# Optimization experiments

Hardware: AMD Instinct MI355X
Metric: run time of the kernel (lower is better)

Reference implementation:

```python
import jax, jax.numpy as jnp
import numpy as np

N_TOKENS = 16384  # b * seq_len
D_MODEL = 4096
NUM_EXPERTS = 64
TOP_K = 2
EPS = 1e-8


def setup_inputs() -> dict:
    key = jax.random.key(0)
    kx, kw = jax.random.split(key)
    x = jax.random.normal(kx, (N_TOKENS, D_MODEL), dtype=jnp.float32)
    # nn.Linear weight: [num_experts, d_model], scaled like torch default init
    W = jax.random.normal(kw, (NUM_EXPERTS, D_MODEL), dtype=jnp.float32) / jnp.sqrt(D_MODEL)
    return {"x": x, "W": W}


def reference(x, W):
    # logits: [n_tokens, num_experts]
    logits = jnp.einsum('nd,ed->ne', x, W)
    scores = jax.nn.softmax(logits, axis=-1)
    topk_scores, topk_indices = jax.lax.top_k(scores, TOP_K)
    topk_scores = topk_scores / jnp.sum(topk_scores, axis=-1, keepdims=True)
    expert_prob = jnp.mean(scores, axis=0)  # [num_experts]
    load_balancing_loss = jnp.sum(expert_prob * jnp.log(expert_prob + EPS))
    return topk_scores, topk_indices, load_balancing_loss
```

## Files before the change

kernel.cpp:

```cpp
#include <hip/hip_runtime.h>
#include <hip/hip_bf16.h>

#define NT 16384
#define DM 4096
#define NE 64
#define MB 64
#define BK 128
#define NST (DM / BK)
#define LROW 132

typedef __attribute__((ext_vector_type(8))) short bf16x8;
typedef __attribute__((ext_vector_type(4))) float f32x4;

__device__ __forceinline__ unsigned short bf16_rne(float f) {
  const unsigned u = __float_as_uint(f);
  return (unsigned short)((u + 0x7FFFu + ((u >> 16) & 1u)) >> 16);
}

__device__ __forceinline__ void split2(float fa, float fb, unsigned& hp, unsigned& lp) {
  union { __hip_bfloat162 h; unsigned u; } cv;
  cv.h = __float22bfloat162_rn(make_float2(fa, fb));
  hp = cv.u;
  const float ha = __uint_as_float(hp << 16);
  const float hb = __uint_as_float(hp & 0xFFFF0000u);
  cv.h = __float22bfloat162_rn(make_float2(fa - ha, fb - hb));
  lp = cv.u;
}

__device__ __forceinline__ void splitA(const float4& c0, const float4& c1,
                                       bf16x8& hi, bf16x8& lo) {
  union { unsigned u[4]; bf16x8 v; } H, L;
  split2(c0.x, c0.y, H.u[0], L.u[0]);
  split2(c0.z, c0.w, H.u[1], L.u[1]);
  split2(c1.x, c1.y, H.u[2], L.u[2]);
  split2(c1.z, c1.w, H.u[3], L.u[3]);
  hi = H.v; lo = L.v;
}

__global__ void w_convert(const float* __restrict__ W,
                          unsigned short* __restrict__ Whi,
                          unsigned short* __restrict__ Wlo) {
  const int id   = blockIdx.x * 256 + threadIdx.x;
  const int lane = id & 63;
  const int nt   = (id >> 6) & 3;
  const int ks   = id >> 8;
  const float* src = W + (size_t)(nt * 16 + (lane & 15)) * DM + ks * 32 + (lane >> 4) * 8;
  unsigned short h[8], l[8];
#pragma unroll
  for (int j = 0; j < 8; ++j) {
    const float f = src[j];
    h[j] = bf16_rne(f);
    l[j] = bf16_rne(f - __uint_as_float((unsigned)h[j] << 16));
  }
  uint4 ph, pl;
  ph.x = h[0] | ((unsigned)h[1] << 16); ph.y = h[2] | ((unsigned)h[3] << 16);
  ph.z = h[4] | ((unsigned)h[5] << 16); ph.w = h[6] | ((unsigned)h[7] << 16);
  pl.x = l[0] | ((unsigned)l[1] << 16); pl.y = l[2] | ((unsigned)l[3] << 16);
  pl.z = l[4] | ((unsigned)l[5] << 16); pl.w = l[6] | ((unsigned)l[7] << 16);
  *(uint4*)(Whi + (size_t)id * 8) = ph;
  *(uint4*)(Wlo + (size_t)id * 8) = pl;
}

__launch_bounds__(512, 2)
__global__ void moe_mfma(const float* __restrict__ x,
                         const unsigned short* __restrict__ Whi,
                         const unsigned short* __restrict__ Wlo,
                         float* __restrict__ out,
                         float* __restrict__ bsum) {
  __shared__ float xs[2][MB][LROW];
  __shared__ float esums[8][NE];
  float* lg = &xs[0][0][0];

  const int tid  = threadIdx.x;
  const int lane = tid & 63;
  const int wv   = tid >> 6;
  const int wvu  = __builtin_amdgcn_readfirstlane(wv);
  const int tg   = wvu >> 1;
  const int eg   = wvu & 1;
  const int blk  = blockIdx.x;
  const int tok0 = blk * MB;

  const int srow = tid >> 3;
  const int scol = (tid & 7) * 4;
  const float* xrow = x + (size_t)(tok0 + srow) * DM + scol;

  float4 g0, g1, g2, g3;
#define LOADSTAGE(s) {                                        \
    const float* p = xrow + (size_t)(s) * BK;                 \
    g0 = *(const float4*)(p);                                 \
    g1 = *(const float4*)(p + 32);                            \
    g2 = *(const float4*)(p + 64);                            \
    g3 = *(const float4*)(p + 96); }
#define WRITESTAGE(b) {                                       \
    float* q = &xs[b][srow][scol];                            \
    *(float4*)(q)      = g0;                                  \
    *(float4*)(q + 32) = g1;                                  \
    *(float4*)(q + 64) = g2;                                  \
    *(float4*)(q + 96) = g3; }

  const unsigned short* bhp = Whi + (size_t)(eg * 2) * 512 + lane * 8;
  const unsigned short* blp = Wlo + (size_t)(eg * 2) * 512 + lane * 8;
  bf16x8 Bh0[2], Bl0[2], Bh1[2], Bl1[2];
#define LOADB(BH, BL, gk) {                                   \
    const size_t o = (size_t)(gk) * 2048;                     \
    BH[0] = *(const bf16x8*)(bhp + o);                        \
    BH[1] = *(const bf16x8*)(bhp + o + 512);                  \
    BL[0] = *(const bf16x8*)(blp + o);                        \
    BL[1] = *(const bf16x8*)(blp + o + 512); }

  const int arow = tg * 16 + (lane & 15);
  const int acol = (lane >> 4) * 8;

  f32x4 acc0 = (f32x4){0.f, 0.f, 0.f, 0.f};
  f32x4 acc1 = (f32x4){0.f, 0.f, 0.f, 0.f};

#define STEP(b, kk, BH, BL) {                                                          \
    const float* ap = &xs[b][arow][acol + (kk) * 32];                                  \
    const float4 f0 = *(const float4*)(ap);                                            \
    const float4 f1 = *(const float4*)(ap + 4);                                        \
    bf16x8 ah, al;                                                                     \
    splitA(f0, f1, ah, al);                                                            \
    acc0 = __builtin_amdgcn_mfma_f32_16x16x32_bf16(al, BL[0], acc0, 0, 0, 0);          \
    acc0 = __builtin_amdgcn_mfma_f32_16x16x32_bf16(al, BH[0], acc0, 0, 0, 0);          \
    acc0 = __builtin_amdgcn_mfma_f32_16x16x32_bf16(ah, BL[0], acc0, 0, 0, 0);          \
    acc0 = __builtin_amdgcn_mfma_f32_16x16x32_bf16(ah, BH[0], acc0, 0, 0, 0);          \
    acc1 = __builtin_amdgcn_mfma_f32_16x16x32_bf16(al, BL[1], acc1, 0, 0, 0);          \
    acc1 = __builtin_amdgcn_mfma_f32_16x16x32_bf16(al, BH[1], acc1, 0, 0, 0);          \
    acc1 = __builtin_amdgcn_mfma_f32_16x16x32_bf16(ah, BL[1], acc1, 0, 0, 0);          \
    acc1 = __builtin_amdgcn_mfma_f32_16x16x32_bf16(ah, BH[1], acc1, 0, 0, 0); }

  LOADSTAGE(0);
  LOADB(Bh0, Bl0, 0);
  WRITESTAGE(0);
  __syncthreads();

  for (int s = 0; s < NST; ++s) {
    const int b = s & 1;
    if (s + 1 < NST) LOADSTAGE(s + 1);
    const int g4 = s * 4;
    const int n1 = g4 + 1, n2 = g4 + 2, n3 = g4 + 3;
    const int n4 = (g4 + 4 < 128) ? g4 + 4 : 127;
    LOADB(Bh1, Bl1, n1); STEP(b, 0, Bh0, Bl0);
    LOADB(Bh0, Bl0, n2); STEP(b, 1, Bh1, Bl1);
    LOADB(Bh1, Bl1, n3); STEP(b, 2, Bh0, Bl0);
    LOADB(Bh0, Bl0, n4); STEP(b, 3, Bh1, Bl1);
    if (s + 1 < NST) WRITESTAGE((s + 1) & 1);
    __syncthreads();
  }

#pragma unroll
  for (int r = 0; r < 4; ++r) {
    const int t = tg * 16 + (lane >> 4) * 4 + r;
    lg[t * 65 + eg * 32 + (lane & 15)]      = acc0[r];
    lg[t * 65 + eg * 32 + 16 + (lane & 15)] = acc1[r];
  }
  __syncthreads();

  float esum = 0.f;
#pragma unroll
  for (int ti = 0; ti < 8; ++ti) {
    const int t = wvu * 8 + ti;
    const float lgv = lg[t * 65 + lane];

    float m = lgv;
#pragma unroll
    for (int off = 32; off; off >>= 1) m = fmaxf(m, __shfl_xor(m, off, 64));
    const float p = __expf(lgv - m);
    float Z = p;
#pragma unroll
    for (int off = 32; off; off >>= 1) Z += __shfl_xor(Z, off, 64);
    const float s = p / Z;
    esum += s;

    float v1 = s; int i1 = lane;
#pragma unroll
    for (int off = 32; off; off >>= 1) {
      const float ov = __shfl_xor(v1, off, 64);
      const int   oi = __shfl_xor(i1, off, 64);
      if (ov > v1 || (ov == v1 && oi < i1)) { v1 = ov; i1 = oi; }
    }
    float sv = (lane == i1) ? -1.f : s;
    float v2 = sv; int i2 = lane;
#pragma unroll
    for (int off = 32; off; off >>= 1) {
      const float ov = __shfl_xor(v2, off, 64);
      const int   oi = __shfl_xor(i2, off, 64);
      if (ov > v2 || (ov == v2 && oi < i2)) { v2 = ov; i2 = oi; }
    }

    if (lane == 0) {
      const int gt = tok0 + t;
      const float inv = 1.f / (v1 + v2);
      out[2 * gt]              = v1 * inv;
      out[2 * gt + 1]          = v2 * inv;
      out[2 * NT + 2 * gt]     = (float)i1;
      out[2 * NT + 2 * gt + 1] = (float)i2;
    }
  }

  esums[wvu][lane] = esum;
  __syncthreads();
  if (wvu == 0) {
    float tot = 0.f;
#pragma unroll
    for (int w = 0; w < 8; ++w) tot += esums[w][lane];
    bsum[blk * NE + lane] = tot;
  }
}

__global__ void moe_gate_loss(const float* __restrict__ bsum,
                              float* __restrict__ out) {
  __shared__ float red[4][64];
  const int e = threadIdx.x & 63;
  const int g = threadIdx.x >> 6;
  float s = 0.f;
  for (int b = g; b < NT / MB; b += 4) s += bsum[b * 64 + e];
  red[g][e] = s;
  __syncthreads();
  if (threadIdx.x < 64) {
    const float tot = red[0][e] + red[1][e] + red[2][e] + red[3][e];
    const float p = tot * (1.f / (float)NT);
    float term = p * logf(p + 1e-8f);
#pragma unroll
    for (int off = 32; off; off >>= 1) term += __shfl_xor(term, off, 64);
    if (e == 0) out[4 * NT] = term;
  }
}

extern "C" void kernel_launch(void* const* d_in, const int* in_sizes, int n_in,
                              void* d_out, int out_size, void* d_ws, size_t ws_size,
                              hipStream_t stream) {
  const float* x = (const float*)d_in[0];
  const float* W = (const float*)d_in[1];
  float* out = (float*)d_out;

  unsigned short* Whi = (unsigned short*)d_ws;
  unsigned short* Wlo = Whi + (size_t)NE * DM;
  float* bsum = (float*)(Wlo + (size_t)NE * DM);

  hipLaunchKernelGGL(w_convert, dim3(128), dim3(256), 0, stream, W, Whi, Wlo);
  hipLaunchKernelGGL(moe_mfma, dim3(NT / MB), dim3(512), 0, stream, x, Whi, Wlo, out, bsum);
  hipLaunchKernelGGL(moe_gate_loss, dim3(1), dim3(256), 0, stream, bsum, out);
}
```

Measured before the change: 106.0 us.

## Split K across waves and stream A directly from global into registers

Each block now handles 32 tokens, and its 8 waves split the K dimension four ways, each wave computing partial logits for 32 tokens × 32 experts. The partials are reduced through shared memory before the softmax. A tiles are loaded straight from global memory into registers with a triple-buffered register pipeline, which removes the LDS staging and the per-stage __syncthreads. Occupancy is raised to 4 blocks per CU and the grid doubles. The cost is more register pressure, uncoalesced-ish per-lane row loads of x, and an extra cross-wave reduction.

```diff
diff --git a/kernel.cpp b/kernel.cpp
--- a/kernel.cpp
+++ b/kernel.cpp
@@ -4,10 +4,10 @@
 #define NT 16384
 #define DM 4096
 #define NE 64
-#define MB 64
-#define BK 128
-#define NST (DM / BK)
-#define LROW 132
+#define MB 32
+#define KG 4
+#define KSW (DM / KG)
+#define KST (KSW / 32)
 
 typedef __attribute__((ext_vector_type(8))) short bf16x8;
 typedef __attribute__((ext_vector_type(4))) float f32x4;
@@ -61,106 +61,100 @@
   *(uint4*)(Wlo + (size_t)id * 8) = pl;
 }
 
-__launch_bounds__(512, 2)
+#define LDA(s, idx) {                                            \
+    const int _o = (idx) * 32;                                   \
+    s##a = *(const float4*)(a0p + _o);                           \
+    s##b = *(const float4*)(a0p + _o + 4);                       \
+    s##c = *(const float4*)(a1p + _o);                           \
+    s##d = *(const float4*)(a1p + _o + 4); }
+
+#define LDB(s, idx) {                                            \
+    const size_t _o = (size_t)(idx) * 2048;                      \
+    s##h0 = *(const bf16x8*)(bhp + _o);                          \
+    s##h1 = *(const bf16x8*)(bhp + _o + 512);                    \
+    s##l0 = *(const bf16x8*)(blp + _o);                          \
+    s##l1 = *(const bf16x8*)(blp + _o + 512); }
+
+#define CMP(sa, sb) {                                                                  \
+    bf16x8 ah0, al0, ah1, al1;                                                         \
+    splitA(sa##a, sa##b, ah0, al0);                                                    \
+    splitA(sa##c, sa##d, ah1, al1);                                                    \
+    acc00 = __builtin_amdgcn_mfma_f32_16x16x32_bf16(al0, sb##l0, acc00, 0, 0, 0);      \
+    acc00 = __builtin_amdgcn_mfma_f32_16x16x32_bf16(al0, sb##h0, acc00, 0, 0, 0);      \
+    acc00 = __builtin_amdgcn_mfma_f32_16x16x32_bf16(ah0, sb##l0, acc00, 0, 0, 0);      \
+    acc00 = __builtin_amdgcn_mfma_f32_16x16x32_bf16(ah0, sb##h0, acc00, 0, 0, 0);      \
+    acc01 = __builtin_amdgcn_mfma_f32_16x16x32_bf16(al0, sb##l1, acc01, 0, 0, 0);      \
+    acc01 = __builtin_amdgcn_mfma_f32_16x16x32_bf16(al0, sb##h1, acc01, 0, 0, 0);      \
+    acc01 = __builtin_amdgcn_mfma_f32_16x16x32_bf16(ah0, sb##l1, acc01, 0, 0, 0);      \
+    acc01 = __builtin_amdgcn_mfma_f32_16x16x32_bf16(ah0, sb##h1, acc01, 0, 0, 0);      \
+    acc10 = __builtin_amdgcn_mfma_f32_16x16x32_bf16(al1, sb##l0, acc10, 0, 0, 0);      \
+    acc10 = __builtin_amdgcn_mfma_f32_16x16x32_bf16(al1, sb##h0, acc10, 0, 0, 0);      \
+    acc10 = __builtin_amdgcn_mfma_f32_16x16x32_bf16(ah1, sb##l0, acc10, 0, 0, 0);      \
+    acc10 = __builtin_amdgcn_mfma_f32_16x16x32_bf16(ah1, sb##h0, acc10, 0, 0, 0);      \
+    acc11 = __builtin_amdgcn_mfma_f32_16x16x32_bf16(al1, sb##l1, acc11, 0, 0, 0);      \
+    acc11 = __builtin_amdgcn_mfma_f32_16x16x32_bf16(al1, sb##h1, acc11, 0, 0, 0);      \
+    acc11 = __builtin_amdgcn_mfma_f32_16x16x32_bf16(ah1, sb##l1, acc11, 0, 0, 0);      \
+    acc11 = __builtin_amdgcn_mfma_f32_16x16x32_bf16(ah1, sb##h1, acc11, 0, 0, 0); }
+
+__launch_bounds__(512, 4)
 __global__ void moe_mfma(const float* __restrict__ x,
                          const unsigned short* __restrict__ Whi,
                          const unsigned short* __restrict__ Wlo,
                          float* __restrict__ out,
                          float* __restrict__ bsum) {
-  __shared__ float xs[2][MB][LROW];
+  __shared__ float lg[KG][MB][NE + 2];
   __shared__ float esums[8][NE];
-  float* lg = &xs[0][0][0];
 
   const int tid  = threadIdx.x;
   const int lane = tid & 63;
-  const int wv   = tid >> 6;
-  const int wvu  = __builtin_amdgcn_readfirstlane(wv);
-  const int tg   = wvu >> 1;
+  const int wvu  = __builtin_amdgcn_readfirstlane(tid >> 6);
   const int eg   = wvu & 1;
+  const int kg   = wvu >> 1;
   const int blk  = blockIdx.x;
   const int tok0 = blk * MB;
 
-  const int srow = tid >> 3;
-  const int scol = (tid & 7) * 4;
-  const float* xrow = x + (size_t)(tok0 + srow) * DM + scol;
-
-  float4 g0, g1, g2, g3;
-#define LOADSTAGE(s) {                                        \
-    const float* p = xrow + (size_t)(s) * BK;                 \
-    g0 = *(const float4*)(p);                                 \
-    g1 = *(const float4*)(p + 32);                            \
-    g2 = *(const float4*)(p + 64);                            \
-    g3 = *(const float4*)(p + 96); }
-#define WRITESTAGE(b) {                                       \
-    float* q = &xs[b][srow][scol];                            \
-    *(float4*)(q)      = g0;                                  \
-    *(float4*)(q + 32) = g1;                                  \
-    *(float4*)(q + 64) = g2;                                  \
-    *(float4*)(q + 96) = g3; }
-
-  const unsigned short* bhp = Whi + (size_t)(eg * 2) * 512 + lane * 8;
-  const unsigned short* blp = Wlo + (size_t)(eg * 2) * 512 + lane * 8;
-  bf16x8 Bh0[2], Bl0[2], Bh1[2], Bl1[2];
-#define LOADB(BH, BL, gk) {                                   \
-    const size_t o = (size_t)(gk) * 2048;                     \
-    BH[0] = *(const bf16x8*)(bhp + o);                        \
-    BH[1] = *(const bf16x8*)(bhp + o + 512);                  \
-    BL[0] = *(const bf16x8*)(blp + o);                        \
-    BL[1] = *(const bf16x8*)(blp + o + 512); }
-
-  const int arow = tg * 16 + (lane & 15);
-  const int acol = (lane >> 4) * 8;
-
-  f32x4 acc0 = (f32x4){0.f, 0.f, 0.f, 0.f};
-  f32x4 acc1 = (f32x4){0.f, 0.f, 0.f, 0.f};
-
-#define STEP(b, kk, BH, BL) {                                                          \
-    const float* ap = &xs[b][arow][acol + (kk) * 32];                                  \
-    const float4 f0 = *(const float4*)(ap);                                            \
-    const float4 f1 = *(const float4*)(ap + 4);                                        \
-    bf16x8 ah, al;                                                                     \
-    splitA(f0, f1, ah, al);                                                            \
-    acc0 = __builtin_amdgcn_mfma_f32_16x16x32_bf16(al, BL[0], acc0, 0, 0, 0);          \
-    acc0 = __builtin_amdgcn_mfma_f32_16x16x32_bf16(al, BH[0], acc0, 0, 0, 0);          \
-    acc0 = __builtin_amdgcn_mfma_f32_16x16x32_bf16(ah, BL[0], acc0, 0, 0, 0);          \
-    acc0 = __builtin_amdgcn_mfma_f32_16x16x32_bf16(ah, BH[0], acc0, 0, 0, 0);          \
-    acc1 = __builtin_amdgcn_mfma_f32_16x16x32_bf16(al, BL[1], acc1, 0, 0, 0);          \
-    acc1 = __builtin_amdgcn_mfma_f32_16x16x32_bf16(al, BH[1], acc1, 0, 0, 0);          \
-    acc1 = __builtin_amdgcn_mfma_f32_16x16x32_bf16(ah, BL[1], acc1, 0, 0, 0);          \
-    acc1 = __builtin_amdgcn_mfma_f32_16x16x32_bf16(ah, BH[1], acc1, 0, 0, 0); }
-
-  LOADSTAGE(0);
-  LOADB(Bh0, Bl0, 0);
-  WRITESTAGE(0);
+  const float* a0p = x + (size_t)(tok0 + (lane & 15)) * DM + kg * KSW + (lane >> 4) * 8;
+  const float* a1p = a0p + (size_t)16 * DM;
+  const unsigned short* bhp = Whi + (size_t)(kg * KST) * 2048 + (size_t)(2 * eg) * 512 + lane * 8;
+  const unsigned short* blp = Wlo + (size_t)(kg * KST) * 2048 + (size_t)(2 * eg) * 512 + lane * 8;
+
+  f32x4 acc00 = (f32x4){0.f, 0.f, 0.f, 0.f};
+  f32x4 acc01 = (f32x4){0.f, 0.f, 0.f, 0.f};
+  f32x4 acc10 = (f32x4){0.f, 0.f, 0.f, 0.f};
+  f32x4 acc11 = (f32x4){0.f, 0.f, 0.f, 0.f};
+
+  float4 A0a, A0b, A0c, A0d, A1a, A1b, A1c, A1d, A2a, A2b, A2c, A2d;
+  bf16x8 B0h0, B0h1, B0l0, B0l1, B1h0, B1h1, B1l0, B1l1;
+
+  LDA(A0, 0); LDA(A1, 1); LDA(A2, 2);
+  LDB(B0, 0); LDB(B1, 1);
+
+  for (int i = 0; i < 30; i += 6) {
+    CMP(A0, B0); LDA(A0, i + 3);          LDB(B0, i + 2);
+    CMP(A1, B1); LDA(A1, i + 4);          LDB(B1, i + 3);
+    CMP(A2, B0); LDA(A2, i + 5);          LDB(B0, i + 4);
+    CMP(A0, B1); LDA(A0, i + 6);          LDB(B1, i + 5);
+    CMP(A1, B0); LDA(A1, min(i + 7, 31)); LDB(B0, i + 6);
+    CMP(A2, B1); LDA(A2, min(i + 8, 31)); LDB(B1, min(i + 7, 31));
+  }
+  CMP(A0, B0);
+  CMP(A1, B1);
+
+#pragma unroll
+  for (int r = 0; r < 4; ++r) {
+    const int tr = (lane >> 4) * 4 + r;
+    lg[kg][tr][eg * 32 + (lane & 15)]           = acc00[r];
+    lg[kg][tr][eg * 32 + 16 + (lane & 15)]      = acc01[r];
+    lg[kg][16 + tr][eg * 32 + (lane & 15)]      = acc10[r];
+    lg[kg][16 + tr][eg * 32 + 16 + (lane & 15)] = acc11[r];
+  }
   __syncthreads();
 
-  for (int s = 0; s < NST; ++s) {
-    const int b = s & 1;
-    if (s + 1 < NST) LOADSTAGE(s + 1);
-    const int g4 = s * 4;
-    const int n1 = g4 + 1, n2 = g4 + 2, n3 = g4 + 3;
-    const int n4 = (g4 + 4 < 128) ? g4 + 4 : 127;
-    LOADB(Bh1, Bl1, n1); STEP(b, 0, Bh0, Bl0);
-    LOADB(Bh0, Bl0, n2); STEP(b, 1, Bh1, Bl1);
-    LOADB(Bh1, Bl1, n3); STEP(b, 2, Bh0, Bl0);
-    LOADB(Bh0, Bl0, n4); STEP(b, 3, Bh1, Bl1);
-    if (s + 1 < NST) WRITESTAGE((s + 1) & 1);
-    __syncthreads();
-  }
-
-#pragma unroll
-  for (int r = 0; r < 4; ++r) {
-    const int t = tg * 16 + (lane >> 4) * 4 + r;
-    lg[t * 65 + eg * 32 + (lane & 15)]      = acc0[r];
-    lg[t * 65 + eg * 32 + 16 + (lane & 15)] = acc1[r];
-  }
-  __syncthreads();
-
   float esum = 0.f;
 #pragma unroll
-  for (int ti = 0; ti < 8; ++ti) {
-    const int t = wvu * 8 + ti;
-    const float lgv = lg[t * 65 + lane];
+  for (int ti = 0; ti < 4; ++ti) {
+    const int t = 4 * wvu + ti;
+    const float lgv = lg[0][t][lane] + lg[1][t][lane] + lg[2][t][lane] + lg[3][t][lane];
 
     float m = lgv;
 #pragma unroll
```

Result: slower. 295.0 us (+178.2%).
